# Kernel tuning notes

Hardware: AMD Instinct MI355X
Metric: run time of the kernel (lower is better)

Reference implementation:

```python
import jax, jax.numpy as jnp
import numpy as np
import math

D_MODEL = 1024
N_HEADS = 16
D_HID = 64
B, L = 2, 2048
NEG = -1e9
EPS = 1e-5


def setup_inputs() -> dict:
    key = jax.random.key(0)
    ks = jax.random.split(key, 16)
    dmh = N_HEADS * D_HID
    s_in = 1.0 / math.sqrt(D_MODEL)
    s_out = 1.0 / math.sqrt(dmh)
    return {
        "Q": jax.random.normal(ks[0], (B, L, D_MODEL), jnp.float32),
        "K": jax.random.normal(ks[1], (B, L, D_MODEL), jnp.float32),
        "V": jax.random.normal(ks[2], (B, L, D_MODEL), jnp.float32),
        "atten_mask": jax.random.randint(ks[3], (B, L, L), 0, 2) > 0,
        "Wq": jax.random.normal(ks[4], (D_MODEL, dmh), jnp.float32) * s_in,
        "bq": jnp.zeros((dmh,), jnp.float32),
        "Wk": jax.random.normal(ks[5], (D_MODEL, dmh), jnp.float32) * s_in,
        "bk": jnp.zeros((dmh,), jnp.float32),
        "Wv": jax.random.normal(ks[6], (D_MODEL, dmh), jnp.float32) * s_in,
        "bv": jnp.zeros((dmh,), jnp.float32),
        "Wo": jax.random.normal(ks[7], (dmh, D_MODEL), jnp.float32) * s_out,
        "bo": jnp.zeros((D_MODEL,), jnp.float32),
        "gamma": jnp.ones((D_MODEL,), jnp.float32),
        "beta": jnp.zeros((D_MODEL,), jnp.float32),
    }


def reference(Q, K, V, atten_mask, Wq, bq, Wk, bk, Wv, bv, Wo, bo, gamma, beta):
    b = Q.shape[0]
    # project and split heads: [B, L, H, Dh] -> [B, H, L, Dh]
    q = (Q @ Wq + bq).reshape(b, -1, N_HEADS, D_HID).transpose(0, 2, 1, 3)
    k = (K @ Wk + bk).reshape(b, -1, N_HEADS, D_HID).transpose(0, 2, 1, 3)
    v = (V @ Wv + bv).reshape(b, -1, N_HEADS, D_HID).transpose(0, 2, 1, 3)
    scale = 1.0 / math.sqrt(D_HID)
    scores = jnp.einsum("bhqd,bhkd->bhqk", q, k * scale)
    scores = jnp.where(atten_mask[:, None, :, :], NEG, scores)
    atten = jax.nn.softmax(scores, axis=-1)
    context = jnp.einsum("bhqk,bhkd->bhqd", atten, v)
    context = context.transpose(0, 2, 1, 3).reshape(b, -1, N_HEADS * D_HID)
    out = context @ Wo + bo
    # residual + LayerNorm
    x = out + Q
    mu = jnp.mean(x, axis=-1, keepdims=True)
    var = jnp.var(x, axis=-1, keepdims=True)
    y = (x - mu) * jax.lax.rsqrt(var + EPS) * gamma + beta
    return (y, atten)
```

## Files before the change

kernel.cpp:

```cpp
#include <hip/hip_runtime.h>
#include <hip/hip_fp16.h>

typedef unsigned short u16;
typedef __attribute__((ext_vector_type(8))) _Float16 f16x8;
typedef __attribute__((ext_vector_type(2))) _Float16 f16x2;
typedef __attribute__((ext_vector_type(4))) float   f32x4;

typedef const __attribute__((address_space(1))) void* gas1_t;
typedef __attribute__((address_space(3))) void*       las3_t;

#define LOG2E 1.44269504089f
#define M12   17.3123404907f

__device__ __forceinline__ void async_ld16(const void* g, void* s){
  __builtin_amdgcn_global_load_lds((gas1_t)g, (las3_t)s, 16, 0, 0);
}
__device__ __forceinline__ u16 f2h(float f){
  return __half_as_ushort(__float2half(f));
}

__global__ void cvt3_kernel(const float* __restrict__ s0, const float* __restrict__ s1,
                            const float* __restrict__ s2, u16* __restrict__ d0,
                            u16* __restrict__ d1, u16* __restrict__ d2)
{
  const float* s = (blockIdx.y==0)? s0 : (blockIdx.y==1)? s1 : s2;
  u16* d = (blockIdx.y==0)? d0 : (blockIdx.y==1)? d1 : d2;
  for(int i = blockIdx.x*256 + threadIdx.x; i < 1048576; i += 512*256){
    float4 v = ((const float4*)s)[i];
    ushort4 o; o.x=f2h(v.x); o.y=f2h(v.y); o.z=f2h(v.z); o.w=f2h(v.w);
    ((ushort4*)d)[i] = o;
  }
}

__global__ void transcvt_kernel(const float* __restrict__ W0, const float* __restrict__ W1,
                                const float* __restrict__ W2, const float* __restrict__ W3,
                                u16* __restrict__ T0, u16* __restrict__ T1,
                                u16* __restrict__ T2, u16* __restrict__ T3)
{
  __shared__ float tile[64][65];
  int z = blockIdx.z;
  const float* W = (z==0)?W0:(z==1)?W1:(z==2)?W2:W3;
  u16* T = (z==0)?T0:(z==1)?T1:(z==2)?T2:T3;
  int k0 = blockIdx.y*64, n0v = blockIdx.x*64;
  int t = threadIdx.x, r = t>>4, c4 = (t&15)*4;
#pragma unroll
  for(int p=0;p<4;p++){
    int rr = p*16 + r;
    float4 v = *(const float4*)&W[(size_t)(k0+rr)*1024 + n0v + c4];
    tile[rr][c4+0]=v.x; tile[rr][c4+1]=v.y; tile[rr][c4+2]=v.z; tile[rr][c4+3]=v.w;
  }
  __syncthreads();
#pragma unroll
  for(int p=0;p<4;p++){
    int rr = p*16 + r;
    ushort4 o;
    o.x = f2h(tile[c4+0][rr]); o.y = f2h(tile[c4+1][rr]);
    o.z = f2h(tile[c4+2][rr]); o.w = f2h(tile[c4+3][rr]);
    *(ushort4*)&T[(size_t)(n0v+rr)*1024 + k0 + c4] = o;
  }
}

__global__ void mask_detect_kernel(const unsigned int* __restrict__ m, int* __restrict__ flag){
  __shared__ int any;
  if(threadIdx.x==0) any = 0;
  __syncthreads();
  int bad = 0;
  for(int i=threadIdx.x;i<2048;i+=256) if(m[i] > 1u) bad = 1;
  if(bad) any = 1;
  __syncthreads();
  if(threadIdx.x==0) *flag = any;
}

__global__ void mask_bits_kernel(const void* __restrict__ msrc, const int* __restrict__ flag,
                                 unsigned long long* __restrict__ mbits)
{
  int gw = (blockIdx.x*256 + threadIdx.x)>>6;
  int lane = threadIdx.x & 63;
  int f = *flag;
  for(int c=0;c<32;c++){
    int idx = gw*2048 + c*64 + lane;
    unsigned v = f ? (unsigned)((const unsigned char*)msrc)[idx]
                   : ((const unsigned int*)msrc)[idx];
    unsigned long long bal = __ballot(v != 0u);
    if(lane==0) mbits[gw*32 + c] = bal;
  }
}

__device__ __forceinline__ void gemm_kloop(const u16* __restrict__ A, const u16* __restrict__ BT,
                                           int m0, int n0, u16* lA, u16* lB, f32x4 acc[4][4])
{
  int t = threadIdx.x, w = t>>6, l = t&63, l4 = l>>4, lm = l&15;
  int wr = w>>1, wc = w&1;
  for(int k0=0;k0<1024;k0+=32){
#pragma unroll
    for(int j=0;j<2;j++){
      int idx = j*4096 + w*1024 + l*16;
      int r = idx>>6, cb = idx&63;
      int cbs = cb ^ ((r&3)<<4);
      async_ld16((const char*)A  + (((size_t)(m0+r))<<11) + k0*2 + cbs,
                 (char*)lA + j*4096 + w*1024);
      async_ld16((const char*)BT + (((size_t)(n0+r))<<11) + k0*2 + cbs,
                 (char*)lB + j*4096 + w*1024);
    }
    __syncthreads();
    f16x8 af[4], bfr[4];
#pragma unroll
    for(int m=0;m<4;m++){
      int ar = wr*64 + m*16 + lm;
      af[m] = *(const f16x8*)((const char*)lA + ar*64 + ((l4*16) ^ ((ar&3)<<4)));
    }
#pragma unroll
    for(int n=0;n<4;n++){
      int br = wc*64 + n*16 + lm;
      bfr[n] = *(const f16x8*)((const char*)lB + br*64 + ((l4*16) ^ ((br&3)<<4)));
    }
#pragma unroll
    for(int m=0;m<4;m++)
#pragma unroll
      for(int n=0;n<4;n++)
        acc[m][n] = __builtin_amdgcn_mfma_f32_16x16x32_f16(af[m], bfr[n], acc[m][n], 0,0,0);
    __syncthreads();
  }
}

__global__ __launch_bounds__(256) void proj_gemm(
    const u16* __restrict__ Xq, const u16* __restrict__ Xk, const u16* __restrict__ Xv,
    const u16* __restrict__ WqT, const u16* __restrict__ WkT, const u16* __restrict__ WvT,
    const float* __restrict__ bq, const float* __restrict__ bk, const float* __restrict__ bv,
    u16* __restrict__ qb, u16* __restrict__ kbuf, u16* __restrict__ vTb)
{
  __shared__ u16 lA[4096], lB[4096];
  int z = blockIdx.z;
  const u16* A  = (z==0)?Xq :(z==1)?Xk :Xv;
  const u16* BT = (z==0)?WqT:(z==1)?WkT:WvT;
  const float* bias = (z==0)?bq:(z==1)?bk:bv;
  int m0 = blockIdx.y*128, n0 = blockIdx.x*128;
  f32x4 zf = {0.f,0.f,0.f,0.f};
  f32x4 acc[4][4];
#pragma unroll
  for(int m=0;m<4;m++)
#pragma unroll
    for(int n=0;n<4;n++) acc[m][n]=zf;
  gemm_kloop(A, BT, m0, n0, lA, lB, acc);

  int t = threadIdx.x, w = t>>6, l = t&63, l4 = l>>4, lm = l&15;
  int wr = w>>1, wc = w&1;
  float scale = (z==1)? 0.125f : 1.0f;
#pragma unroll
  for(int n=0;n<4;n++){
    int ng = n0 + wc*64 + n*16 + lm;
    float bsv = bias[ng];
#pragma unroll
    for(int m=0;m<4;m++){
      int mb = m0 + wr*64 + m*16 + l4*4;
      f32x4 c = acc[m][n];
      int bhh = ((mb>>11)<<4) + (ng>>6);
      if(z<2){
        u16* dst = (z==0)? qb : kbuf;
        size_t base = (((size_t)bhh)<<17) + ((size_t)(mb&2047)<<6) + (ng&63);
        dst[base      ] = f2h((c[0]+bsv)*scale);
        dst[base +  64] = f2h((c[1]+bsv)*scale);
        dst[base + 128] = f2h((c[2]+bsv)*scale);
        dst[base + 192] = f2h((c[3]+bsv)*scale);
      } else {
        size_t off = (((size_t)bhh)<<17) + ((size_t)(ng&63)<<11) + (mb&2047);
        ushort4 o;
        o.x=f2h(c[0]+bsv); o.y=f2h(c[1]+bsv); o.z=f2h(c[2]+bsv); o.w=f2h(c[3]+bsv);
        *(ushort4*)(vTb + off) = o;
      }
    }
  }
}

__global__ __launch_bounds__(256) void attn_fused(
    const u16* __restrict__ qb, const u16* __restrict__ kb,
    const u16* __restrict__ vTb, const unsigned long long* __restrict__ mbits,
    float* __restrict__ att, u16* __restrict__ ctx)
{
  __shared__ u16 ktile[4096];
  __shared__ u16 vtile[4096];
  __shared__ u16 pl[4][16*136];
  int bh = blockIdx.y, b = bh>>4, h = bh&15;
  int q0 = blockIdx.x*64;
  int t = threadIdx.x, w = t>>6, l = t&63, l4 = l>>4, lm = l&15;
  int qw = q0 + w*16 + lm;

  const u16* qrow = qb + ((size_t)bh*2048 + qw)*64;
  f16x8 qB0 = *(const f16x8*)(qrow + l4*8);
  f16x8 qB1 = *(const f16x8*)(qrow + 32 + l4*8);

  const unsigned long long* mrow = mbits + (size_t)(b*2048 + qw)*32;
  const char* kbase_b = (const char*)(kb  + ((size_t)bh<<17));
  const char* vbase_b = (const char*)(vTb + ((size_t)bh<<17));
  f32x4 zf = {0.f,0.f,0.f,0.f};

  float esum = 0.f;
  for(int kt=0;kt<32;kt++){
    int gk = kt*64;
#pragma unroll
    for(int j=0;j<2;j++){
      int idx = j*4096 + t*16, row = idx>>7, cb = idx&127;
      async_ld16(kbase_b + (size_t)(gk+row)*128 + (cb ^ ((row&7)<<4)),
                 (char*)ktile + idx);
    }
    __syncthreads();
    unsigned long long mw = mrow[kt];
    unsigned mlo = (unsigned)mw, mhi = (unsigned)(mw>>32);
#pragma unroll
    for(int kf=0;kf<4;kf++){
      int keyr = kf*16 + lm, sw = (keyr&7)<<4;
      const char* kp = (const char*)ktile + keyr*128;
      f16x8 a0 = *(const f16x8*)(kp + ((l4*16) ^ sw));
      f16x8 a1 = *(const f16x8*)(kp + ((64 + l4*16) ^ sw));
      f32x4 s = __builtin_amdgcn_mfma_f32_16x16x32_f16(a0, qB0, zf, 0,0,0);
      s = __builtin_amdgcn_mfma_f32_16x16x32_f16(a1, qB1, s, 0,0,0);
      unsigned nib = (((kf&2)?mhi:mlo) >> ((kf&1)*16 + l4*4)) & 15u;
      esum += exp2f(((nib&1u)? -1e9f : s[0])*LOG2E - M12);
      esum += exp2f(((nib&2u)? -1e9f : s[1])*LOG2E - M12);
      esum += exp2f(((nib&4u)? -1e9f : s[2])*LOG2E - M12);
      esum += exp2f(((nib&8u)? -1e9f : s[3])*LOG2E - M12);
    }
    __syncthreads();
  }
  esum += __shfl_xor(esum, 16);
  esum += __shfl_xor(esum, 32);
  float lrs = -M12 - log2f(fmaxf(esum, 1e-30f));

  f32x4 cacc[4] = {zf,zf,zf,zf};
  int q_hi = l>>5, koff = (l&31)*4;
  float* abase = att + ((size_t)bh*2048 + q0 + w*16)*2048;
  u16* plw = &pl[w][0];

  for(int kg=0; kg<16; kg++){
#pragma unroll
    for(int km=0; km<2; km++){
      int kt = kg*2 + km, gk = kt*64;
#pragma unroll
      for(int j=0;j<2;j++){
        int idx = j*4096 + t*16, row = idx>>7, cb = idx&127;
        async_ld16(kbase_b + (size_t)(gk+row)*128 + (cb ^ ((row&7)<<4)),
                   (char*)ktile + idx);
        async_ld16(vbase_b + (size_t)row*4096 + gk*2 + (cb ^ ((row&7)<<4)),
                   (char*)vtile + idx);
      }
      __syncthreads();
      unsigned long long mw = mrow[kt];
      unsigned mlo = (unsigned)mw, mhi = (unsigned)(mw>>32);
#pragma unroll
      for(int kf=0;kf<4;kf++){
        int keyr = kf*16 + lm, sw = (keyr&7)<<4;
        const char* kp = (const char*)ktile + keyr*128;
        f16x8 a0 = *(const f16x8*)(kp + ((l4*16) ^ sw));
        f16x8 a1 = *(const f16x8*)(kp + ((64 + l4*16) ^ sw));
        f32x4 s = __builtin_amdgcn_mfma_f32_16x16x32_f16(a0, qB0, zf, 0,0,0);
        s = __builtin_amdgcn_mfma_f32_16x16x32_f16(a1, qB1, s, 0,0,0);
        unsigned nib = (((kf&2)?mhi:mlo) >> ((kf&1)*16 + l4*4)) & 15u;
        float p0 = exp2f(((nib&1u)? -1e9f : s[0])*LOG2E + lrs);
        float p1 = exp2f(((nib&2u)? -1e9f : s[1])*LOG2E + lrs);
        float p2 = exp2f(((nib&4u)? -1e9f : s[2])*LOG2E + lrs);
        float p3 = exp2f(((nib&8u)? -1e9f : s[3])*LOG2E + lrs);
        uint2 pk;
        pk.x = __builtin_bit_cast(unsigned, __builtin_amdgcn_cvt_pkrtz(p0,p1));
        pk.y = __builtin_bit_cast(unsigned, __builtin_amdgcn_cvt_pkrtz(p2,p3));
        *(uint2*)(plw + lm*136 + km*64 + kf*16 + l4*4) = pk;
      }
#pragma unroll
      for(int kk=0;kk<2;kk++){
        f16x8 pb = *(const f16x8*)(plw + lm*136 + km*64 + kk*32 + l4*8);
#pragma unroll
        for(int mf=0;mf<4;mf++){
          int dr = mf*16 + lm;
          const char* vp = (const char*)vtile + dr*128;
          f16x8 av = *(const f16x8*)(vp + ((kk*64 + l4*16) ^ ((dr&7)<<4)));
          cacc[mf] = __builtin_amdgcn_mfma_f32_16x16x32_f16(av, pb, cacc[mf], 0,0,0);
        }
      }
      __syncthreads();
    }
#pragma unroll
    for(int qq=0; qq<16; qq+=2){
      int q = qq + q_hi;
      uint2 ph = *(const uint2*)(plw + q*136 + koff);
      f16x2 h0 = __builtin_bit_cast(f16x2, ph.x);
      f16x2 h1 = __builtin_bit_cast(f16x2, ph.y);
      f32x4 o4 = { (float)h0[0], (float)h0[1], (float)h1[0], (float)h1[1] };
      __builtin_nontemporal_store(o4,
          (f32x4*)(abase + (size_t)q*2048 + kg*128 + koff));
    }
  }
  int token = b*2048 + qw;
#pragma unroll
  for(int mf=0;mf<4;mf++){
    ushort4 o;
    o.x=f2h(cacc[mf][0]); o.y=f2h(cacc[mf][1]);
    o.z=f2h(cacc[mf][2]); o.w=f2h(cacc[mf][3]);
    *(ushort4*)(ctx + (size_t)token*1024 + h*64 + mf*16 + l4*4) = o;
  }
}

__global__ __launch_bounds__(256) void out_gemm(
    const u16* __restrict__ ctx, const u16* __restrict__ WoT,
    const float* __restrict__ bo, const float* __restrict__ Qres, float* __restrict__ xout)
{
  __shared__ u16 lA[4096], lB[4096];
  int m0 = blockIdx.y*128, n0 = blockIdx.x*128;
  f32x4 zf = {0.f,0.f,0.f,0.f};
  f32x4 acc[4][4];
#pragma unroll
  for(int m=0;m<4;m++)
#pragma unroll
    for(int n=0;n<4;n++) acc[m][n]=zf;
  gemm_kloop(ctx, WoT, m0, n0, lA, lB, acc);

  int t = threadIdx.x, w = t>>6, l = t&63, l4 = l>>4, lm = l&15;
  int wr = w>>1, wc = w&1;
#pragma unroll
  for(int n=0;n<4;n++){
    int ng = n0 + wc*64 + n*16 + lm;
    float bsv = bo[ng];
#pragma unroll
    for(int m=0;m<4;m++){
      int mb = m0 + wr*64 + m*16 + l4*4;
      f32x4 c = acc[m][n];
#pragma unroll
      for(int j=0;j<4;j++){
        size_t o = ((size_t)(mb+j)<<10) + ng;
        xout[o] = c[j] + bsv + Qres[o];
      }
    }
  }
}

__global__ void ln_kernel(const float* __restrict__ x, const float* __restrict__ gamma,
                          const float* __restrict__ beta, float* __restrict__ y)
{
  int row = blockIdx.x, t = threadIdx.x;
  float4 v = ((const float4*)(x + (size_t)row*1024))[t];
  float s  = v.x+v.y+v.z+v.w;
  float sq = v.x*v.x + v.y*v.y + v.z*v.z + v.w*v.w;
#pragma unroll
  for(int d=1; d<64; d<<=1){ s += __shfl_xor(s, d); sq += __shfl_xor(sq, d); }
  __shared__ float red[8];
  int w = t>>6, l = t&63;
  if(l==0){ red[w] = s; red[4+w] = sq; }
  __syncthreads();
  s  = red[0]+red[1]+red[2]+red[3];
  sq = red[4]+red[5]+red[6]+red[7];
  float mu  = s * 0.0009765625f;
  float var = sq * 0.0009765625f - mu*mu;
  float rs  = rsqrtf(var + 1e-5f);
  float4 g  = ((const float4*)gamma)[t];
  float4 be = ((const float4*)beta)[t];
  float4 o;
  o.x = (v.x-mu)*rs*g.x + be.x;
  o.y = (v.y-mu)*rs*g.y + be.y;
  o.z = (v.z-mu)*rs*g.z + be.z;
  o.w = (v.w-mu)*rs*g.w + be.w;
  ((float4*)(y + (size_t)row*1024))[t] = o;
}

extern "C" void kernel_launch(void* const* d_in, const int* in_sizes, int n_in,
                              void* d_out, int out_size, void* d_ws, size_t ws_size,
                              hipStream_t stream)
{
  (void)in_sizes; (void)n_in; (void)out_size; (void)ws_size;
  const float* Q    = (const float*)d_in[0];
  const float* K    = (const float*)d_in[1];
  const float* V    = (const float*)d_in[2];
  const void*  mraw = d_in[3];
  const float* Wq   = (const float*)d_in[4];
  const float* bq   = (const float*)d_in[5];
  const float* Wk   = (const float*)d_in[6];
  const float* bk   = (const float*)d_in[7];
  const float* Wv   = (const float*)d_in[8];
  const float* bv   = (const float*)d_in[9];
  const float* Wo   = (const float*)d_in[10];
  const float* bo   = (const float*)d_in[11];
  const float* gamma= (const float*)d_in[12];
  const float* beta = (const float*)d_in[13];

  char* ws = (char*)d_ws;
  const size_t MB = 1ull<<20;
  u16* WqT  = (u16*)(ws + 0*MB);
  u16* WkT  = (u16*)(ws + 2*MB);
  u16* WvT  = (u16*)(ws + 4*MB);
  u16* WoT  = (u16*)(ws + 6*MB);
  u16* Xq   = (u16*)(ws + 8*MB);
  u16* Xk   = (u16*)(ws + 16*MB);
  u16* Xv   = (u16*)(ws + 24*MB);
  u16* qb   = (u16*)(ws + 32*MB);
  u16* kbuf = (u16*)(ws + 40*MB);
  u16* vTb  = (u16*)(ws + 48*MB);
  u16* ctx  = (u16*)(ws + 56*MB);
  unsigned long long* mbits = (unsigned long long*)(ws + 8*MB);
  int* flag = (int*)(ws + 10*MB);
  float* xres = (float*)(ws + 16*MB);

  float* yout = (float*)d_out;
  float* att  = (float*)d_out + 4194304;

  cvt3_kernel<<<dim3(512,3,1), 256, 0, stream>>>(Q,K,V,Xq,Xk,Xv);
  transcvt_kernel<<<dim3(16,16,4), 256, 0, stream>>>(Wq,Wk,Wv,Wo,WqT,WkT,WvT,WoT);
  proj_gemm<<<dim3(8,32,3), 256, 0, stream>>>(Xq,Xk,Xv,WqT,WkT,WvT,bq,bk,bv,qb,kbuf,vTb);
  mask_detect_kernel<<<1,256,0,stream>>>((const unsigned int*)mraw, flag);
  mask_bits_kernel<<<1024,256,0,stream>>>(mraw, flag, mbits);
  attn_fused<<<dim3(32,32), 256, 0, stream>>>(qb,kbuf,vTb,mbits,att,ctx);
  out_gemm<<<dim3(8,32), 256, 0, stream>>>(ctx,WoT,bo,Q,xres);
  ln_kernel<<<4096, 256, 0, stream>>>(xres,gamma,beta,yout);
}
```

Measured before the change: 270.5 us.

## Double-buffer LDS tiles in GEMMs and attention; widen attention blocks to 512 threads

Both GEMM k-loops and both attention passes now use two LDS buffers, so the async load of the next K/V or A/B tile is issued before the current one is computed, removing one barrier per iteration. The attention kernel goes to 512 threads per block covering 128 queries, which halves the grid and shares each K/V tile across twice as many queries. It also raises wave priority around the MFMA sections. The cost is doubled LDS use, which may reduce occupancy. It also relies on the single remaining barrier per iteration being enough to keep the asynchronous loads from racing with reads of the other buffer.

New measurement: 277.7 us. 2.7% more time.

```diff
diff --git a/kernel.cpp b/kernel.cpp
--- a/kernel.cpp
+++ b/kernel.cpp
@@ -91,28 +91,34 @@
 {
   int t = threadIdx.x, w = t>>6, l = t&63, l4 = l>>4, lm = l&15;
   int wr = w>>1, wc = w&1;
-  for(int k0=0;k0<1024;k0+=32){
+  auto STAGE = [&](int k0, int half){
 #pragma unroll
     for(int j=0;j<2;j++){
       int idx = j*4096 + w*1024 + l*16;
       int r = idx>>6, cb = idx&63;
       int cbs = cb ^ ((r&3)<<4);
       async_ld16((const char*)A  + (((size_t)(m0+r))<<11) + k0*2 + cbs,
-                 (char*)lA + j*4096 + w*1024);
+                 (char*)lA + half*8192 + j*4096 + w*1024);
       async_ld16((const char*)BT + (((size_t)(n0+r))<<11) + k0*2 + cbs,
-                 (char*)lB + j*4096 + w*1024);
-    }
-    __syncthreads();
+                 (char*)lB + half*8192 + j*4096 + w*1024);
+    }
+  };
+  STAGE(0, 0);
+  __syncthreads();
+  for(int kt=0; kt<32; kt++){
+    if(kt<31) STAGE((kt+1)*32, (kt+1)&1);
+    const char* pA = (const char*)lA + (kt&1)*8192;
+    const char* pB = (const char*)lB + (kt&1)*8192;
     f16x8 af[4], bfr[4];
 #pragma unroll
     for(int m=0;m<4;m++){
       int ar = wr*64 + m*16 + lm;
-      af[m] = *(const f16x8*)((const char*)lA + ar*64 + ((l4*16) ^ ((ar&3)<<4)));
+      af[m] = *(const f16x8*)(pA + ar*64 + ((l4*16) ^ ((ar&3)<<4)));
     }
 #pragma unroll
     for(int n=0;n<4;n++){
       int br = wc*64 + n*16 + lm;
-      bfr[n] = *(const f16x8*)((const char*)lB + br*64 + ((l4*16) ^ ((br&3)<<4)));
+      bfr[n] = *(const f16x8*)(pB + br*64 + ((l4*16) ^ ((br&3)<<4)));
     }
 #pragma unroll
     for(int m=0;m<4;m++)
@@ -129,7 +135,7 @@
     const float* __restrict__ bq, const float* __restrict__ bk, const float* __restrict__ bv,
     u16* __restrict__ qb, u16* __restrict__ kbuf, u16* __restrict__ vTb)
 {
-  __shared__ u16 lA[4096], lB[4096];
+  __shared__ u16 lA[8192], lB[8192];
   int z = blockIdx.z;
   const u16* A  = (z==0)?Xq :(z==1)?Xk :Xv;
   const u16* BT = (z==0)?WqT:(z==1)?WkT:WvT;
@@ -172,16 +178,16 @@
   }
 }
 
-__global__ __launch_bounds__(256) void attn_fused(
+__global__ __launch_bounds__(512, 4) void attn_fused(
     const u16* __restrict__ qb, const u16* __restrict__ kb,
     const u16* __restrict__ vTb, const unsigned long long* __restrict__ mbits,
     float* __restrict__ att, u16* __restrict__ ctx)
 {
-  __shared__ u16 ktile[4096];
-  __shared__ u16 vtile[4096];
-  __shared__ u16 pl[4][16*136];
+  __shared__ u16 kdb[2][4096];
+  __shared__ u16 vdb[2][4096];
+  __shared__ u16 pl[8][16*136];
   int bh = blockIdx.y, b = bh>>4, h = bh&15;
-  int q0 = blockIdx.x*64;
+  int q0 = blockIdx.x*128;
   int t = threadIdx.x, w = t>>6, l = t&63, l4 = l>>4, lm = l&15;
   int qw = q0 + w*16 + lm;
 
@@ -194,22 +200,29 @@
   const char* vbase_b = (const char*)(vTb + ((size_t)bh<<17));
   f32x4 zf = {0.f,0.f,0.f,0.f};
 
+  int srow = t>>3, scb = (t&7)*16;
+  auto STAGE_K = [&](int kt, int half){
+    async_ld16(kbase_b + (size_t)(kt*64+srow)*128 + (scb ^ ((srow&7)<<4)),
+               (char*)kdb[half] + t*16);
+  };
+  auto STAGE_V = [&](int kt, int half){
+    async_ld16(vbase_b + (size_t)srow*4096 + kt*128 + (scb ^ ((srow&7)<<4)),
+               (char*)vdb[half] + t*16);
+  };
+
   float esum = 0.f;
+  STAGE_K(0,0);
+  __syncthreads();
   for(int kt=0;kt<32;kt++){
-    int gk = kt*64;
-#pragma unroll
-    for(int j=0;j<2;j++){
-      int idx = j*4096 + t*16, row = idx>>7, cb = idx&127;
-      async_ld16(kbase_b + (size_t)(gk+row)*128 + (cb ^ ((row&7)<<4)),
-                 (char*)ktile + idx);
-    }
-    __syncthreads();
+    if(kt<31) STAGE_K(kt+1, (kt+1)&1);
+    const char* kbuf_h = (const char*)kdb[kt&1];
     unsigned long long mw = mrow[kt];
     unsigned mlo = (unsigned)mw, mhi = (unsigned)(mw>>32);
+    __builtin_amdgcn_s_setprio(1);
 #pragma unroll
     for(int kf=0;kf<4;kf++){
       int keyr = kf*16 + lm, sw = (keyr&7)<<4;
-      const char* kp = (const char*)ktile + keyr*128;
+      const char* kp = kbuf_h + keyr*128;
       f16x8 a0 = *(const f16x8*)(kp + ((l4*16) ^ sw));
       f16x8 a1 = *(const f16x8*)(kp + ((64 + l4*16) ^ sw));
       f32x4 s = __builtin_amdgcn_mfma_f32_16x16x32_f16(a0, qB0, zf, 0,0,0);
@@ -220,6 +233,7 @@
       esum += exp2f(((nib&4u)? -1e9f : s[2])*LOG2E - M12);
       esum += exp2f(((nib&8u)? -1e9f : s[3])*LOG2E - M12);
     }
+    __builtin_amdgcn_s_setprio(0);
     __syncthreads();
   }
   esum += __shfl_xor(esum, 16);
@@ -231,25 +245,22 @@
   float* abase = att + ((size_t)bh*2048 + q0 + w*16)*2048;
   u16* plw = &pl[w][0];
 
+  STAGE_K(0,0); STAGE_V(0,0);
+  __syncthreads();
   for(int kg=0; kg<16; kg++){
 #pragma unroll
     for(int km=0; km<2; km++){
-      int kt = kg*2 + km, gk = kt*64;
-#pragma unroll
-      for(int j=0;j<2;j++){
-        int idx = j*4096 + t*16, row = idx>>7, cb = idx&127;
-        async_ld16(kbase_b + (size_t)(gk+row)*128 + (cb ^ ((row&7)<<4)),
-                   (char*)ktile + idx);
-        async_ld16(vbase_b + (size_t)row*4096 + gk*2 + (cb ^ ((row&7)<<4)),
-                   (char*)vtile + idx);
-      }
-      __syncthreads();
+      int kt = kg*2 + km;
+      if(kt<31){ STAGE_K(kt+1,(kt+1)&1); STAGE_V(kt+1,(kt+1)&1); }
+      const char* kbuf_h = (const char*)kdb[kt&1];
+      const char* vbuf_h = (const char*)vdb[kt&1];
       unsigned long long mw = mrow[kt];
       unsigned mlo = (unsigned)mw, mhi = (unsigned)(mw>>32);
+      __builtin_amdgcn_s_setprio(1);
 #pragma unroll
       for(int kf=0;kf<4;kf++){
         int keyr = kf*16 + lm, sw = (keyr&7)<<4;
-        const char* kp = (const char*)ktile + keyr*128;
+        const char* kp = kbuf_h + keyr*128;
         f16x8 a0 = *(const f16x8*)(kp + ((l4*16) ^ sw));
         f16x8 a1 = *(const f16x8*)(kp + ((64 + l4*16) ^ sw));
         f32x4 s = __builtin_amdgcn_mfma_f32_16x16x32_f16(a0, qB0, zf, 0,0,0);
@@ -270,11 +281,12 @@
 #pragma unroll
         for(int mf=0;mf<4;mf++){
           int dr = mf*16 + lm;
-          const char* vp = (const char*)vtile + dr*128;
+          const char* vp = vbuf_h + dr*128;
           f16x8 av = *(const f16x8*)(vp + ((kk*64 + l4*16) ^ ((dr&7)<<4)));
           cacc[mf] = __builtin_amdgcn_mfma_f32_16x16x32_f16(av, pb, cacc[mf], 0,0,0);
         }
       }
+      __builtin_amdgcn_s_setprio(0);
       __syncthreads();
     }
 #pragma unroll
@@ -302,7 +314,7 @@
     const u16* __restrict__ ctx, const u16* __restrict__ WoT,
     const float* __restrict__ bo, const float* __restrict__ Qres, float* __restrict__ xout)
 {
-  __shared__ u16 lA[4096], lB[4096];
+  __shared__ u16 lA[8192], lB[8192];
   int m0 = blockIdx.y*128, n0 = blockIdx.x*128;
   f32x4 zf = {0.f,0.f,0.f,0.f};
   f32x4 acc[4][4];
@@ -404,7 +416,7 @@
   proj_gemm<<<dim3(8,32,3), 256, 0, stream>>>(Xq,Xk,Xv,WqT,WkT,WvT,bq,bk,bv,qb,kbuf,vTb);
   mask_detect_kernel<<<1,256,0,stream>>>((const unsigned int*)mraw, flag);
   mask_bits_kernel<<<1024,256,0,stream>>>(mraw, flag, mbits);
-  attn_fused<<<dim3(32,32), 256, 0, stream>>>(qb,kbuf,vTb,mbits,att,ctx);
+  attn_fused<<<dim3(16,32), 512, 0, stream>>>(qb,kbuf,vTb,mbits,att,ctx);
   out_gemm<<<dim3(8,32), 256, 0, stream>>>(ctx,WoT,bo,Q,xres);
   ln_kernel<<<4096, 256, 0, stream>>>(xres,gamma,beta,yout);
 }
```

## Split attention into key-split row-sum and PV passes with partial reduction

Applied to the files above, without the earlier changes.

The single fused attention kernel becomes two kernels. The first computes softmax denominators over four key splits, giving 4x more blocks. The second computes normalized probabilities and the PV product over two key halves, writing partial fp16 context buffers that a small reduction kernel then sums. The aim is more blocks in flight on the GPU, since the original grid had only 1024 blocks, each walking all 2048 keys twice. In exchange it adds extra launches, partial-buffer traffic, and fp16 rounding of partial context sums.

Result: slower. 292.7 us (+8.2%).

```diff
diff --git a/kernel.cpp b/kernel.cpp
--- a/kernel.cpp
+++ b/kernel.cpp
@@ -172,30 +172,25 @@
   }
 }
 
-__global__ __launch_bounds__(256) void attn_fused(
+__global__ __launch_bounds__(256) void attn_sums(
     const u16* __restrict__ qb, const u16* __restrict__ kb,
-    const u16* __restrict__ vTb, const unsigned long long* __restrict__ mbits,
-    float* __restrict__ att, u16* __restrict__ ctx)
+    const unsigned long long* __restrict__ mbits, float* __restrict__ rsum_part)
 {
   __shared__ u16 ktile[4096];
-  __shared__ u16 vtile[4096];
-  __shared__ u16 pl[4][16*136];
-  int bh = blockIdx.y, b = bh>>4, h = bh&15;
-  int q0 = blockIdx.x*64;
+  int bh = blockIdx.y, b = bh>>4, qt = blockIdx.x, ks = blockIdx.z;
   int t = threadIdx.x, w = t>>6, l = t&63, l4 = l>>4, lm = l&15;
-  int qw = q0 + w*16 + lm;
+  int qw = qt*64 + w*16 + lm;
 
   const u16* qrow = qb + ((size_t)bh*2048 + qw)*64;
   f16x8 qB0 = *(const f16x8*)(qrow + l4*8);
   f16x8 qB1 = *(const f16x8*)(qrow + 32 + l4*8);
 
   const unsigned long long* mrow = mbits + (size_t)(b*2048 + qw)*32;
-  const char* kbase_b = (const char*)(kb  + ((size_t)bh<<17));
-  const char* vbase_b = (const char*)(vTb + ((size_t)bh<<17));
+  const char* kbase_b = (const char*)(kb + ((size_t)bh<<17));
   f32x4 zf = {0.f,0.f,0.f,0.f};
 
   float esum = 0.f;
-  for(int kt=0;kt<32;kt++){
+  for(int kt=ks*8; kt<ks*8+8; kt++){
     int gk = kt*64;
 #pragma unroll
     for(int j=0;j<2;j++){
@@ -224,17 +219,48 @@
   }
   esum += __shfl_xor(esum, 16);
   esum += __shfl_xor(esum, 32);
-  float lrs = -M12 - log2f(fmaxf(esum, 1e-30f));
+  if(l < 16)
+    rsum_part[(size_t)ks*65536 + (size_t)bh*2048 + qw] = esum;
+}
+
+__global__ __launch_bounds__(256) void attn_pv(
+    const u16* __restrict__ qb, const u16* __restrict__ kb,
+    const u16* __restrict__ vTb, const unsigned long long* __restrict__ mbits,
+    const float* __restrict__ rsum_part, float* __restrict__ att, u16* __restrict__ ctxp)
+{
+  __shared__ u16 ktile[4096];
+  __shared__ u16 vtile[4096];
+  __shared__ u16 pl[4][16*136];
+  int bh = blockIdx.y, b = bh>>4, h = bh&15;
+  int qt = blockIdx.x, ks = blockIdx.z;
+  int q0 = qt*64;
+  int t = threadIdx.x, w = t>>6, l = t&63, l4 = l>>4, lm = l&15;
+  int qw = q0 + w*16 + lm;
+
+  const u16* qrow = qb + ((size_t)bh*2048 + qw)*64;
+  f16x8 qB0 = *(const f16x8*)(qrow + l4*8);
+  f16x8 qB1 = *(const f16x8*)(qrow + 32 + l4*8);
+
+  size_t rbase = (size_t)bh*2048 + qw;
+  float S = rsum_part[rbase] + rsum_part[65536+rbase]
+          + rsum_part[131072+rbase] + rsum_part[196608+rbase];
+  float lrs = -M12 - log2f(fmaxf(S, 1e-30f));
+
+  const unsigned long long* mrow = mbits + (size_t)(b*2048 + qw)*32;
+  const char* kbase_b = (const char*)(kb  + ((size_t)bh<<17));
+  const char* vbase_b = (const char*)(vTb + ((size_t)bh<<17));
+  f32x4 zf = {0.f,0.f,0.f,0.f};
 
   f32x4 cacc[4] = {zf,zf,zf,zf};
   int q_hi = l>>5, koff = (l&31)*4;
   float* abase = att + ((size_t)bh*2048 + q0 + w*16)*2048;
   u16* plw = &pl[w][0];
 
-  for(int kg=0; kg<16; kg++){
+  for(int kg=0; kg<8; kg++){
+    int kt0 = ks*16 + kg*2;
 #pragma unroll
     for(int km=0; km<2; km++){
-      int kt = kg*2 + km, gk = kt*64;
+      int kt = kt0 + km, gk = kt*64;
 #pragma unroll
       for(int j=0;j<2;j++){
         int idx = j*4096 + t*16, row = idx>>7, cb = idx&127;
@@ -285,17 +311,26 @@
       f16x2 h1 = __builtin_bit_cast(f16x2, ph.y);
       f32x4 o4 = { (float)h0[0], (float)h0[1], (float)h1[0], (float)h1[1] };
       __builtin_nontemporal_store(o4,
-          (f32x4*)(abase + (size_t)q*2048 + kg*128 + koff));
+          (f32x4*)(abase + (size_t)q*2048 + kt0*64 + koff));
     }
   }
   int token = b*2048 + qw;
+  u16* cp = ctxp + (size_t)ks*4194304 + (size_t)token*1024 + h*64;
 #pragma unroll
   for(int mf=0;mf<4;mf++){
     ushort4 o;
     o.x=f2h(cacc[mf][0]); o.y=f2h(cacc[mf][1]);
     o.z=f2h(cacc[mf][2]); o.w=f2h(cacc[mf][3]);
-    *(ushort4*)(ctx + (size_t)token*1024 + h*64 + mf*16 + l4*4) = o;
-  }
+    *(ushort4*)(cp + mf*16 + l4*4) = o;
+  }
+}
+
+__global__ void ctx_reduce(const u16* __restrict__ ctxp, u16* __restrict__ ctx){
+  int i = blockIdx.x*256 + threadIdx.x;
+  f16x8 a = ((const f16x8*)ctxp)[i];
+  f16x8 b = ((const f16x8*)(ctxp + 4194304))[i];
+  f16x8 s = a + b;
+  ((f16x8*)ctx)[i] = s;
 }
 
 __global__ __launch_bounds__(256) void out_gemm(
@@ -393,7 +428,9 @@
   u16* vTb  = (u16*)(ws + 48*MB);
   u16* ctx  = (u16*)(ws + 56*MB);
   unsigned long long* mbits = (unsigned long long*)(ws + 8*MB);
+  float* rsum_part = (float*)(ws + 9*MB);
   int* flag = (int*)(ws + 10*MB);
+  u16* ctxp = (u16*)(ws + 16*MB);
   float* xres = (float*)(ws + 16*MB);
 
   float* yout = (float*)d_out;
@@ -404,7 +441,9 @@
   proj_gemm<<<dim3(8,32,3), 256, 0, stream>>>(Xq,Xk,Xv,WqT,WkT,WvT,bq,bk,bv,qb,kbuf,vTb);
   mask_detect_kernel<<<1,256,0,stream>>>((const unsigned int*)mraw, flag);
   mask_bits_kernel<<<1024,256,0,stream>>>(mraw, flag, mbits);
-  attn_fused<<<dim3(32,32), 256, 0, stream>>>(qb,kbuf,vTb,mbits,att,ctx);
+  attn_sums<<<dim3(32,32,4), 256, 0, stream>>>(qb, kbuf, mbits, rsum_part);
+  attn_pv<<<dim3(32,32,2), 256, 0, stream>>>(qb,kbuf,vTb,mbits,rsum_part,att,ctxp);
+  ctx_reduce<<<2048, 256, 0, stream>>>(ctxp, ctx);
   out_gemm<<<dim3(8,32), 256, 0, stream>>>(ctx,WoT,bo,Q,xres);
   ln_kernel<<<4096, 256, 0, stream>>>(xres,gamma,beta,yout);
 }
```
